# Kernel tuning notes

Hardware: AMD Instinct MI355X
Metric: run time of the kernel (lower is better)

Reference implementation:

```python
import jax, jax.numpy as jnp
import numpy as np

B, T, C, H, HS = 128, 256, 384, 6, 64
DFF = 4 * C
EPS = 1e-5


def layer_norm(x, g, b):
    mu = jnp.mean(x, axis=-1, keepdims=True)
    var = jnp.mean(jnp.square(x - mu), axis=-1, keepdims=True)
    return (x - mu) * jax.lax.rsqrt(var + EPS) * g + b


def setup_inputs() -> dict:
    key = jax.random.key(0)
    ks = jax.random.split(key, 12)
    s_in = 1.0 / np.sqrt(C)
    s_ff = 1.0 / np.sqrt(DFF)
    return {
        "x": jax.random.normal(ks[0], (B, T, C), jnp.float32),
        "Wq": jax.random.normal(ks[1], (H, C, HS), jnp.float32) * s_in,
        "Wk": jax.random.normal(ks[2], (H, C, HS), jnp.float32) * s_in,
        "Wv": jax.random.normal(ks[3], (H, C, HS), jnp.float32) * s_in,
        "Wo": jax.random.normal(ks[4], (C, C), jnp.float32) * s_in,
        "bo": jnp.zeros((C,), jnp.float32),
        "W1": jax.random.normal(ks[5], (C, DFF), jnp.float32) * s_in,
        "b1": jnp.zeros((DFF,), jnp.float32),
        "W2": jax.random.normal(ks[6], (DFF, C), jnp.float32) * s_ff,
        "b2": jnp.zeros((C,), jnp.float32),
        "g1": jnp.ones((C,), jnp.float32),
        "be1": jnp.zeros((C,), jnp.float32),
        "g2": jnp.ones((C,), jnp.float32),
        "be2": jnp.zeros((C,), jnp.float32),
    }


def reference(x, Wq, Wk, Wv, Wo, bo, W1, b1, W2, b2, g1, be1, g2, be2):
    # --- pre-norm causal multi-head self-attention (dropout = identity, eval mode) ---
    h = layer_norm(x, g1, be1)                      # (B,T,C)
    q = jnp.einsum('btc,hcd->bhtd', h, Wq)          # (B,H,T,HS)
    k = jnp.einsum('btc,hcd->bhtd', h, Wk)
    v = jnp.einsum('btc,hcd->bhtd', h, Wv)
    scale = HS ** -0.5
    wei = jnp.einsum('bhtd,bhsd->bhts', q, k) * scale   # (B,H,T,T)
    causal = jnp.tril(jnp.ones((T, T), bool))
    wei = jnp.where(causal, wei, -jnp.inf)
    wei = jax.nn.softmax(wei, axis=-1)
    attn = jnp.einsum('bhts,bhsd->bhtd', wei, v)         # (B,H,T,HS)
    attn = attn.transpose(0, 2, 1, 3).reshape(x.shape[0], x.shape[1], C)  # concat heads
    sa = attn @ Wo + bo
    x = x + sa
    # --- pre-norm FFN ---
    h2 = layer_norm(x, g2, be2)
    ff = jax.nn.relu(h2 @ W1 + b1) @ W2 + b2
    return x + ff
```

## Files before the change

kernel.cpp:

```cpp
#include <hip/hip_runtime.h>
#include <hip/hip_bf16.h>

#define BB   128
#define TT   256
#define CC   384
#define HH   6
#define HSZ  64
#define DFF  1536
#define EPSV 1e-5f
#define RPB  8
#define NTOK (BB * TT)
#define NQKV (3 * CC)

typedef __attribute__((ext_vector_type(8))) short  short8;
typedef __attribute__((ext_vector_type(4))) float  f32x4;
typedef __hip_bfloat16 bf16;

__device__ __forceinline__ void async_copy16(const bf16* g, bf16* l) {
    __builtin_amdgcn_global_load_lds(
        (const __attribute__((address_space(1))) void*)g,
        (__attribute__((address_space(3))) void*)l, 16, 0, 0);
}

__device__ __forceinline__ void block_reduce2(float& a, float& b, float* red) {
    #pragma unroll
    for (int off = 32; off > 0; off >>= 1) {
        a += __shfl_down(a, off, 64);
        b += __shfl_down(b, off, 64);
    }
    const int lane = threadIdx.x & 63;
    const int wid  = threadIdx.x >> 6;
    if (lane == 0) { red[wid * 2] = a; red[wid * 2 + 1] = b; }
    __syncthreads();
    if (threadIdx.x == 0) {
        float sa = 0.f, sb = 0.f;
        #pragma unroll
        for (int w = 0; w < 6; ++w) { sa += red[w * 2]; sb += red[w * 2 + 1]; }
        red[12] = sa; red[13] = sb;
    }
    __syncthreads();
    a = red[12]; b = red[13];
}

__global__ __launch_bounds__(CC) void ln_bf16_kernel(
        const float* __restrict__ x, const float* __restrict__ g,
        const float* __restrict__ be, bf16* __restrict__ y) {
    __shared__ float red[16];
    const int tid = threadIdx.x;
    const long row0 = (long)blockIdx.x * RPB;
    const float gg = g[tid], bb = be[tid];
    for (int r = 0; r < RPB; ++r) {
        float v = x[(row0 + r) * CC + tid];
        float s = v, sq = v * v;
        block_reduce2(s, sq, red);
        float mu  = s  * (1.0f / CC);
        float var = sq * (1.0f / CC) - mu * mu;
        float rs  = rsqrtf(var + EPSV);
        y[(row0 + r) * CC + tid] = __float2bfloat16((v - mu) * rs * gg + bb);
        __syncthreads();
    }
}

__global__ __launch_bounds__(256) void pack_weights(
        const float* __restrict__ Wq, const float* __restrict__ Wk,
        const float* __restrict__ Wv, const float* __restrict__ Wo,
        const float* __restrict__ W1, const float* __restrict__ W2,
        bf16* __restrict__ WcatT, bf16* __restrict__ WoT,
        bf16* __restrict__ W1T, bf16* __restrict__ W2T) {
    __shared__ float t[32][33];
    const int id = blockIdx.x;
    const float* in; bf16* out; int R, Cn, c0, r0;
    if (id < 432) {
        const int which = id / 144, rem = id % 144, h = rem / 24, tt = rem % 24;
        const float* W = (which == 0) ? Wq : ((which == 1) ? Wk : Wv);
        in = W + (long)h * CC * HSZ;  R = CC; Cn = HSZ;
        c0 = (tt % 2) * 32; r0 = (tt / 2) * 32;
        out = WcatT + ((long)which * CC + h * HSZ) * CC;
    } else if (id < 576) {
        const int i2 = id - 432;
        in = Wo; out = WoT; R = CC; Cn = CC;
        c0 = (i2 % 12) * 32; r0 = (i2 / 12) * 32;
    } else if (id < 1152) {
        const int i3 = id - 576;
        in = W1; out = W1T; R = CC; Cn = DFF;
        c0 = (i3 % 48) * 32; r0 = (i3 / 48) * 32;
    } else {
        const int i4 = id - 1152;
        in = W2; out = W2T; R = DFF; Cn = CC;
        c0 = (i4 % 12) * 32; r0 = (i4 / 12) * 32;
    }
    const int tid = threadIdx.x, tx = tid & 31, ty = tid >> 5;
    #pragma unroll
    for (int p = 0; p < 4; ++p)
        t[ty + p * 8][tx] = in[(long)(r0 + ty + p * 8) * Cn + c0 + tx];
    __syncthreads();
    #pragma unroll
    for (int p = 0; p < 4; ++p)
        out[(long)(c0 + ty + p * 8) * R + r0 + tx] = __float2bfloat16(t[tx][ty + p * 8]);
}

template<int K, int EPI>
__global__ __launch_bounds__(512) void gemm_fn(
        const bf16* __restrict__ A, const bf16* __restrict__ BT,
        const float* __restrict__ bias, const float* __restrict__ res,
        float* __restrict__ outF, bf16* __restrict__ outB, int N, int nby) {
    __shared__ bf16 A0[128 * 32];
    __shared__ bf16 A1[128 * 32];
    __shared__ bf16 B0[384 * 32];
    __shared__ bf16 B1[384 * 32];

    const int tid = threadIdx.x;

    const int hwid  = blockIdx.x;
    const int chunk = gridDim.x >> 3;
    const int e     = hwid & 7;
    const int s     = hwid >> 3;
    const int gx    = chunk / nby;
    const int bx    = e * gx + s / nby;
    const int by    = s - (s / nby) * nby;
    const int m0 = bx * 128;
    const int n0 = by * 384;

    const int ln   = tid & 63;
    const int wid  = tid >> 6;
    const int wm   = (wid & 1) * 64;
    const int wn   = (wid >> 1) * 96;
    const int fr   = ln & 15;
    const int quad = ln >> 4;
    const int slot = quad ^ ((fr >> 1) & 3);

    const int rA = tid >> 2, gA = (tid & 3) ^ ((rA >> 1) & 3);
    const long gaA = (long)rA * K + gA * 8;
    const int uB1 = tid + 512, uB2 = tid + 1024;
    const int rB0 = tid >> 2, gB0 = (tid & 3) ^ ((rB0 >> 1) & 3);
    const int rB1 = uB1 >> 2, gB1 = (uB1 & 3) ^ ((rB1 >> 1) & 3);
    const int rB2 = uB2 >> 2, gB2 = (uB2 & 3) ^ ((rB2 >> 1) & 3);
    const long gaB0 = (long)rB0 * K + gB0 * 8;
    const long gaB1 = (long)rB1 * K + gB1 * 8;
    const long gaB2 = (long)rB2 * K + gB2 * 8;
    const bf16* Ap  = A  + (long)m0 * K;
    const bf16* BTp = BT + (long)n0 * K;

    f32x4 acc[4][6];
    #pragma unroll
    for (int i = 0; i < 4; ++i)
        #pragma unroll
        for (int j = 0; j < 6; ++j)
            acc[i][j] = (f32x4){0.f, 0.f, 0.f, 0.f};

    constexpr int NT = K / 32;
    static_assert(NT % 2 == 0, "2-buffer rotation requires even NT");

    auto stage = [&](long k0, bf16* Ad, bf16* Bd) {
        async_copy16(Ap  + gaA  + k0, Ad + tid * 8);
        async_copy16(BTp + gaB0 + k0, Bd + tid * 8);
        async_copy16(BTp + gaB1 + k0, Bd + uB1 * 8);
        async_copy16(BTp + gaB2 + k0, Bd + uB2 * 8);
    };

    auto phase = [&](int t, bf16* Ab, bf16* Bb) {
        if (t + 1 < NT) {
            asm volatile("s_waitcnt vmcnt(4)" ::: "memory");
        } else {
            asm volatile("s_waitcnt vmcnt(0)" ::: "memory");
        }
        __builtin_amdgcn_s_barrier();

        short8 af[4], bfr[6];
        #pragma unroll
        for (int i = 0; i < 4; ++i)
            af[i] = *(const short8*)(Ab + (wm + i * 16 + fr) * 32 + slot * 8);
        #pragma unroll
        for (int j = 0; j < 6; ++j)
            bfr[j] = *(const short8*)(Bb + (wn + j * 16 + fr) * 32 + slot * 8);
        asm volatile("s_waitcnt lgkmcnt(0)" ::: "memory");
        __builtin_amdgcn_s_barrier();
        __builtin_amdgcn_sched_barrier(0);

        if (t + 2 < NT) stage((long)(t + 2) * 32, Ab, Bb);

        #pragma unroll
        for (int i = 0; i < 4; ++i)
            #pragma unroll
            for (int j = 0; j < 6; ++j)
                acc[i][j] = __builtin_amdgcn_mfma_f32_16x16x32_bf16(
                    af[i], bfr[j], acc[i][j], 0, 0, 0);
    };

    stage(0,  A0, B0);
    stage(32, A1, B1);

    for (int t = 0; t < NT; t += 2) {
        phase(t,     A0, B0);
        phase(t + 1, A1, B1);
    }

    #pragma unroll
    for (int i = 0; i < 4; ++i) {
        #pragma unroll
        for (int j = 0; j < 6; ++j) {
            const int col = n0 + wn + j * 16 + fr;
            #pragma unroll
            for (int r = 0; r < 4; ++r) {
                const int row = m0 + wm + i * 16 + quad * 4 + r;
                const long idx = (long)row * N + col;
                float v = acc[i][j][r];
                if (EPI == 1) {
                    v = fmaxf(v + bias[col], 0.f);
                    outB[idx] = __float2bfloat16(v);
                } else if (EPI == 2) {
                    outF[idx] = v + bias[col] + res[idx];
                } else {
                    outB[idx] = __float2bfloat16(v);
                }
            }
        }
    }
}

struct alignas(8) bh4s { bf16 a, b, c, d; };

__global__ __launch_bounds__(256, 2) void attn_mfma_kernel(
        const bf16* __restrict__ qkv, bf16* __restrict__ ab) {
    __shared__ bf16 Kt[64][72];
    __shared__ bf16 Vt[64][72];
    __shared__ bf16 Pb[4][16][72];

    const int tid  = threadIdx.x;
    const int bh   = blockIdx.x;
    const int b    = bh / HH, h = bh % HH;
    const int w    = tid >> 6;
    const int ln   = tid & 63;
    const int ln15 = ln & 15;
    const int quad = ln >> 4;

    short8 qf[4][2];
    #pragma unroll
    for (int i = 0; i < 4; ++i) {
        const long tok = (long)b * TT + w * 16 + i * 64 + ln15;
        const bf16* p = qkv + tok * NQKV + h * HSZ + quad * 8;
        qf[i][0] = *(const short8*)p;
        qf[i][1] = *(const short8*)(p + 32);
    }

    f32x4 accO[4][4];
    float mrow[4][4], lrow[4][4];
    #pragma unroll
    for (int i = 0; i < 4; ++i) {
        #pragma unroll
        for (int j = 0; j < 4; ++j) accO[i][j] = (f32x4){0.f, 0.f, 0.f, 0.f};
        #pragma unroll
        for (int r = 0; r < 4; ++r) { mrow[i][r] = -1e30f; lrow[i][r] = 0.f; }
    }

    for (int sidx = 0; sidx < 4; ++sidx) {
        const int s0 = sidx * 64;
        __syncthreads();
        {
            const bf16* kg = qkv + (long)(b * TT + s0) * NQKV + CC + h * HSZ;
            #pragma unroll
            for (int it = 0; it < 2; ++it) {
                const int u = tid + it * 256;
                const int r = u >> 3, c = (u & 7) * 8;
                *(uint4*)&Kt[r][c] = *(const uint4*)(kg + (long)r * NQKV + c);
            }
            const bf16* vg = qkv + (long)(b * TT + s0) * NQKV + 2 * CC + h * HSZ;
            const int s = tid & 63;
            #pragma unroll
            for (int it = 0; it < 4; ++it) {
                const int dq = (tid >> 6) + it * 4;
                const bh4s vv = *(const bh4s*)(vg + (long)s * NQKV + dq * 4);
                Vt[dq * 4 + 0][s] = vv.a;
                Vt[dq * 4 + 1][s] = vv.b;
                Vt[dq * 4 + 2][s] = vv.c;
                Vt[dq * 4 + 3][s] = vv.d;
            }
        }
        __syncthreads();

        #pragma unroll
        for (int i = 0; i < 4; ++i) {
            if (i < sidx) continue;
            const int rb = w * 16 + i * 64;
            f32x4 S[4];
            #pragma unroll
            for (int jt = 0; jt < 4; ++jt) S[jt] = (f32x4){0.f, 0.f, 0.f, 0.f};
            #pragma unroll
            for (int ks = 0; ks < 2; ++ks) {
                #pragma unroll
                for (int jt = 0; jt < 4; ++jt) {
                    const short8 kf = *(const short8*)&Kt[jt * 16 + ln15][ks * 32 + quad * 8];
                    S[jt] = __builtin_amdgcn_mfma_f32_16x16x32_bf16(qf[i][ks], kf, S[jt], 0, 0, 0);
                }
            }
            float rmax[4];
            #pragma unroll
            for (int r = 0; r < 4; ++r) rmax[r] = -1e30f;
            #pragma unroll
            for (int jt = 0; jt < 4; ++jt) {
                #pragma unroll
                for (int r = 0; r < 4; ++r) {
                    float v = S[jt][r] * 0.125f;
                    if (i == sidx) {
                        const int col = s0 + jt * 16 + ln15;
                        const int row = rb + quad * 4 + r;
                        if (col > row) v = -1e30f;
                    }
                    S[jt][r] = v;
                    rmax[r] = fmaxf(rmax[r], v);
                }
            }
            #pragma unroll
            for (int off = 1; off < 16; off <<= 1)
                #pragma unroll
                for (int r = 0; r < 4; ++r)
                    rmax[r] = fmaxf(rmax[r], __shfl_xor(rmax[r], off, 64));

            float alpha[4], rsum[4];
            #pragma unroll
            for (int r = 0; r < 4; ++r) {
                const float mn = fmaxf(mrow[i][r], rmax[r]);
                alpha[r] = __expf(mrow[i][r] - mn);
                mrow[i][r] = mn;
                rsum[r] = 0.f;
            }
            #pragma unroll
            for (int jt = 0; jt < 4; ++jt)
                #pragma unroll
                for (int r = 0; r < 4; ++r) {
                    const float p = __expf(S[jt][r] - mrow[i][r]);
                    S[jt][r] = p;
                    rsum[r] += p;
                }
            #pragma unroll
            for (int off = 1; off < 16; off <<= 1)
                #pragma unroll
                for (int r = 0; r < 4; ++r)
                    rsum[r] += __shfl_xor(rsum[r], off, 64);
            #pragma unroll
            for (int r = 0; r < 4; ++r)
                lrow[i][r] = lrow[i][r] * alpha[r] + rsum[r];
            #pragma unroll
            for (int jt = 0; jt < 4; ++jt)
                #pragma unroll
                for (int r = 0; r < 4; ++r)
                    accO[i][jt][r] *= alpha[r];

            #pragma unroll
            for (int jt = 0; jt < 4; ++jt)
                #pragma unroll
                for (int r = 0; r < 4; ++r)
                    Pb[w][quad * 4 + r][jt * 16 + ln15] = __float2bfloat16(S[jt][r]);
            const short8 pf0 = *(const short8*)&Pb[w][ln15][quad * 8];
            const short8 pf1 = *(const short8*)&Pb[w][ln15][32 + quad * 8];
            #pragma unroll
            for (int jt = 0; jt < 4; ++jt) {
                const short8 vf0 = *(const short8*)&Vt[jt * 16 + ln15][quad * 8];
                const short8 vf1 = *(const short8*)&Vt[jt * 16 + ln15][32 + quad * 8];
                accO[i][jt] = __builtin_amdgcn_mfma_f32_16x16x32_bf16(pf0, vf0, accO[i][jt], 0, 0, 0);
                accO[i][jt] = __builtin_amdgcn_mfma_f32_16x16x32_bf16(pf1, vf1, accO[i][jt], 0, 0, 0);
            }
        }
    }

    #pragma unroll
    for (int i = 0; i < 4; ++i) {
        const int rb = w * 16 + i * 64;
        float inv[4];
        #pragma unroll
        for (int r = 0; r < 4; ++r) inv[r] = 1.0f / lrow[i][r];
        #pragma unroll
        for (int jt = 0; jt < 4; ++jt)
            #pragma unroll
            for (int r = 0; r < 4; ++r)
                Pb[w][quad * 4 + r][jt * 16 + ln15] = __float2bfloat16(accO[i][jt][r] * inv[r]);
        #pragma unroll
        for (int it = 0; it < 2; ++it) {
            const int u = ln + it * 64;
            const int row = u >> 3, ch = (u & 7) * 8;
            const long tok = (long)b * TT + rb + row;
            *(uint4*)(ab + tok * CC + h * HSZ + ch) = *(const uint4*)&Pb[w][row][ch];
        }
    }
}

extern "C" void kernel_launch(void* const* d_in, const int* in_sizes, int n_in,
                              void* d_out, int out_size, void* d_ws, size_t ws_size,
                              hipStream_t stream) {
    const float* x   = (const float*)d_in[0];
    const float* Wq  = (const float*)d_in[1];
    const float* Wk  = (const float*)d_in[2];
    const float* Wv  = (const float*)d_in[3];
    const float* Wo  = (const float*)d_in[4];
    const float* bo  = (const float*)d_in[5];
    const float* W1  = (const float*)d_in[6];
    const float* b1  = (const float*)d_in[7];
    const float* W2  = (const float*)d_in[8];
    const float* b2  = (const float*)d_in[9];
    const float* g1  = (const float*)d_in[10];
    const float* be1 = (const float*)d_in[11];
    const float* g2  = (const float*)d_in[12];
    const float* be2 = (const float*)d_in[13];

    float* out = (float*)d_out;
    char*  ws  = (char*)d_ws;

    const size_t qkvBytes = (size_t)NTOK * NQKV * 4;
    const size_t actOff   = (qkvBytes + 255) & ~(size_t)255;
    const size_t actBytes = (size_t)NTOK * CC * 2;
    size_t wOff = (actOff + actBytes + 255) & ~(size_t)255;

    bf16* qkvb = (bf16*)ws;
    bf16* ff1  = (bf16*)ws;
    bf16* actb = (bf16*)(ws + actOff);

    bf16* WcatT = (bf16*)(ws + wOff); wOff += (size_t)NQKV * CC * 2 + 256;
    bf16* WoT   = (bf16*)(ws + ((wOff + 255) & ~(size_t)255)); wOff = ((wOff + 255) & ~(size_t)255) + (size_t)CC * CC * 2;
    bf16* W1T   = (bf16*)(ws + ((wOff + 255) & ~(size_t)255)); wOff = ((wOff + 255) & ~(size_t)255) + (size_t)DFF * CC * 2;
    bf16* W2T   = (bf16*)(ws + ((wOff + 255) & ~(size_t)255));

    pack_weights<<<1728, 256, 0, stream>>>(Wq, Wk, Wv, Wo, W1, W2,
                                           WcatT, WoT, W1T, W2T);

    ln_bf16_kernel<<<NTOK / RPB, CC, 0, stream>>>(x, g1, be1, actb);
    gemm_fn<CC, 3><<<(NTOK / 128) * 3, 512, 0, stream>>>(
        actb, WcatT, nullptr, nullptr, nullptr, qkvb, NQKV, 3);
    attn_mfma_kernel<<<BB * HH, 256, 0, stream>>>(qkvb, actb);
    gemm_fn<CC, 2><<<(NTOK / 128), 512, 0, stream>>>(
        actb, WoT, bo, x, out, nullptr, CC, 1);

    ln_bf16_kernel<<<NTOK / RPB, CC, 0, stream>>>(out, g2, be2, actb);
    gemm_fn<CC, 1><<<(NTOK / 128) * 4, 512, 0, stream>>>(
        actb, W1T, b1, nullptr, nullptr, ff1, DFF, 4);
    gemm_fn<DFF, 2><<<(NTOK / 128), 512, 0, stream>>>(
        ff1, W2T, b2, out, out, nullptr, CC, 1);
}
```

Baseline: 412.9 us.

## Fuse FFN up- and down-projection GEMMs into one kernel with LDS-resident hidden tile

Replaces the two FFN GEMM launches with one kernel. For each 128-row tile it computes 192-wide chunks of relu(h2·W1+b1), packs them as bf16 into shared memory, and immediately accumulates them into the W2 output with bias and residual. This removes the global write and reread of the large 32768x1536 intermediate and one launch. In exchange the grid is only 256 blocks of 512 threads with heavy LDS use and one block per CU, so occupancy is low and the pipeline schedule is intricate.

```diff
diff --git a/kernel.cpp b/kernel.cpp
--- a/kernel.cpp
+++ b/kernel.cpp
@@ -15,6 +15,11 @@
 typedef __attribute__((ext_vector_type(8))) short  short8;
 typedef __attribute__((ext_vector_type(4))) float  f32x4;
 typedef __hip_bfloat16 bf16;
+
+#define WAITV(n) asm volatile("s_waitcnt vmcnt(" #n ")" ::: "memory")
+#define WAITL    asm volatile("s_waitcnt lgkmcnt(0)" ::: "memory")
+#define BAR      __builtin_amdgcn_s_barrier()
+#define SCHED    __builtin_amdgcn_sched_barrier(0)
 
 __device__ __forceinline__ void async_copy16(const bf16* g, bf16* l) {
     __builtin_amdgcn_global_load_lds(
@@ -110,7 +115,6 @@
     __shared__ bf16 B1[384 * 32];
 
     const int tid = threadIdx.x;
-
     const int hwid  = blockIdx.x;
     const int chunk = gridDim.x >> 3;
     const int e     = hwid & 7;
@@ -149,7 +153,6 @@
             acc[i][j] = (f32x4){0.f, 0.f, 0.f, 0.f};
 
     constexpr int NT = K / 32;
-    static_assert(NT % 2 == 0, "2-buffer rotation requires even NT");
 
     auto stage = [&](long k0, bf16* Ad, bf16* Bd) {
         async_copy16(Ap  + gaA  + k0, Ad + tid * 8);
@@ -159,13 +162,8 @@
     };
 
     auto phase = [&](int t, bf16* Ab, bf16* Bb) {
-        if (t + 1 < NT) {
-            asm volatile("s_waitcnt vmcnt(4)" ::: "memory");
-        } else {
-            asm volatile("s_waitcnt vmcnt(0)" ::: "memory");
-        }
-        __builtin_amdgcn_s_barrier();
-
+        if (t + 1 < NT) { WAITV(4); } else { WAITV(0); }
+        BAR;
         short8 af[4], bfr[6];
         #pragma unroll
         for (int i = 0; i < 4; ++i)
@@ -173,12 +171,10 @@
         #pragma unroll
         for (int j = 0; j < 6; ++j)
             bfr[j] = *(const short8*)(Bb + (wn + j * 16 + fr) * 32 + slot * 8);
-        asm volatile("s_waitcnt lgkmcnt(0)" ::: "memory");
-        __builtin_amdgcn_s_barrier();
-        __builtin_amdgcn_sched_barrier(0);
-
+        WAITL;
+        BAR;
+        SCHED;
         if (t + 2 < NT) stage((long)(t + 2) * 32, Ab, Bb);
-
         #pragma unroll
         for (int i = 0; i < 4; ++i)
             #pragma unroll
@@ -205,14 +201,202 @@
                 const int row = m0 + wm + i * 16 + quad * 4 + r;
                 const long idx = (long)row * N + col;
                 float v = acc[i][j][r];
-                if (EPI == 1) {
-                    v = fmaxf(v + bias[col], 0.f);
-                    outB[idx] = __float2bfloat16(v);
-                } else if (EPI == 2) {
+                if (EPI == 2) {
                     outF[idx] = v + bias[col] + res[idx];
                 } else {
                     outB[idx] = __float2bfloat16(v);
                 }
+            }
+        }
+    }
+}
+
+__global__ __launch_bounds__(512, 1) void ffn_fused(
+        const bf16* __restrict__ A, const bf16* __restrict__ W1T,
+        const bf16* __restrict__ W2T, const float* __restrict__ b1,
+        const float* __restrict__ b2, float* __restrict__ out) {
+    __shared__ bf16 Pl[6 * 128 * 32];
+    __shared__ bf16 Ab0[2 * 128 * 32];
+    __shared__ bf16 Ab1[2 * 128 * 32];
+    __shared__ bf16 Bb0[1536 * 8];
+    __shared__ bf16 Bb1[1536 * 8];
+    __shared__ float b1L[DFF];
+    __shared__ float b2L[CC];
+
+    const int tid  = threadIdx.x;
+    const int hwid = blockIdx.x;
+    const int bx   = (hwid & 7) * 32 + (hwid >> 3);
+    const int m0   = bx * 128;
+
+    const int ln   = tid & 63;
+    const int wid  = tid >> 6;
+    const int wm   = (wid & 1) * 64;
+    const int wn1  = (wid >> 1) * 48;
+    const int wn2  = (wid >> 1) * 96;
+    const int fr   = ln & 15;
+    const int quad = ln >> 4;
+    const int sw8  = (quad ^ ((fr >> 1) & 3)) * 8;
+
+    for (int t = tid; t < DFF; t += 512) b1L[t] = b1[t];
+    for (int t = tid; t < CC;  t += 512) b2L[t] = b2[t];
+
+    const bf16* Ap = A + (long)m0 * CC;
+
+    auto stageA = [&](int s, bf16* Ad) {
+        #pragma unroll
+        for (int p = 0; p < 2; ++p) {
+            const int u = tid + p * 512;
+            const int kk = u >> 9, idx = u & 511;
+            const int row = idx >> 2, g = idx & 3;
+            const int gg = g ^ ((row >> 1) & 3);
+            async_copy16(Ap + (long)row * CC + s * 64 + kk * 32 + gg * 8,
+                         Ad + u * 8);
+        }
+    };
+    auto stageB1 = [&](int dffm, int s, bf16* Bd) {
+        #pragma unroll
+        for (int p = 0; p < 3; ++p) {
+            const int u = tid + p * 512;
+            const int sub = (u >= 768) ? 1 : 0;
+            const int idx = u - sub * 768;
+            const int row = idx >> 2, g = idx & 3;
+            const int gg = g ^ ((row >> 1) & 3);
+            async_copy16(W1T + (long)(dffm + row) * CC + s * 64 + sub * 32 + gg * 8,
+                         Bd + u * 8);
+        }
+    };
+    auto stageB2 = [&](int dffm, int uu, bf16* Bd) {
+        #pragma unroll
+        for (int p = 0; p < 3; ++p) {
+            const int u = tid + p * 512;
+            const int row = u >> 2, g = u & 3;
+            const int gg = g ^ ((row >> 1) & 3);
+            async_copy16(W2T + (long)row * DFF + dffm + uu * 32 + gg * 8,
+                         Bd + u * 8);
+        }
+    };
+
+    f32x4 acc1[4][3], acc2[4][6];
+    #pragma unroll
+    for (int i = 0; i < 4; ++i) {
+        #pragma unroll
+        for (int j = 0; j < 3; ++j) acc1[i][j] = (f32x4){0.f, 0.f, 0.f, 0.f};
+        #pragma unroll
+        for (int j = 0; j < 6; ++j) acc2[i][j] = (f32x4){0.f, 0.f, 0.f, 0.f};
+    }
+
+    auto g1phase = [&](const bf16* Ac, const bf16* Bc, int mode, int dffm,
+                       int aux, bf16* AD, bf16* BD) {
+        short8 af[4][2], bf1[3][2];
+        #pragma unroll
+        for (int kk = 0; kk < 2; ++kk) {
+            #pragma unroll
+            for (int i = 0; i < 4; ++i)
+                af[i][kk] = *(const short8*)(Ac + ((kk << 7) + wm + i * 16 + fr) * 32 + sw8);
+            #pragma unroll
+            for (int j = 0; j < 3; ++j)
+                bf1[j][kk] = *(const short8*)(Bc + (kk * 192 + wn1 + j * 16 + fr) * 32 + sw8);
+        }
+        WAITL;
+        BAR;
+        SCHED;
+        if (mode == 0) { stageA(aux, AD); stageB1(dffm, aux, BD); }
+        else if (mode == 1) { stageB2(dffm, aux, BD); }
+        #pragma unroll
+        for (int kk = 0; kk < 2; ++kk)
+            #pragma unroll
+            for (int i = 0; i < 4; ++i)
+                #pragma unroll
+                for (int j = 0; j < 3; ++j)
+                    acc1[i][j] = __builtin_amdgcn_mfma_f32_16x16x32_bf16(
+                        af[i][kk], bf1[j][kk], acc1[i][j], 0, 0, 0);
+    };
+    auto g2phase = [&](int uu, const bf16* Bc, int mode, int dffm,
+                       int aux, bf16* AD, bf16* BD) {
+        short8 af2[4], bf2[6];
+        #pragma unroll
+        for (int i = 0; i < 4; ++i)
+            af2[i] = *(const short8*)(Pl + (uu * 128 + wm + i * 16 + fr) * 32 + sw8);
+        #pragma unroll
+        for (int j = 0; j < 6; ++j)
+            bf2[j] = *(const short8*)(Bc + (wn2 + j * 16 + fr) * 32 + sw8);
+        WAITL;
+        BAR;
+        SCHED;
+        if (mode == 0) { stageA(aux, AD); stageB1(dffm, aux, BD); }
+        else if (mode == 1) { stageB2(dffm, aux, BD); }
+        #pragma unroll
+        for (int i = 0; i < 4; ++i)
+            #pragma unroll
+            for (int j = 0; j < 6; ++j)
+                acc2[i][j] = __builtin_amdgcn_mfma_f32_16x16x32_bf16(
+                    af2[i], bf2[j], acc2[i][j], 0, 0, 0);
+    };
+
+    __syncthreads();
+
+    stageA(0, Ab0); stageB1(0, 0, Bb0);
+    stageA(1, Ab1); stageB1(0, 1, Bb1);
+
+    for (int cc = 0; cc < 8; ++cc) {
+        const int dff0 = cc * 192;
+        const bool pf  = (cc < 7);
+        const int dffN = dff0 + 192;
+
+        WAITV(5); BAR; g1phase(Ab0, Bb0, 0, dff0, 2, Ab0, Bb0);
+        WAITV(5); BAR; g1phase(Ab1, Bb1, 0, dff0, 3, Ab1, Bb1);
+        WAITV(5); BAR; g1phase(Ab0, Bb0, 0, dff0, 4, Ab0, Bb0);
+        WAITV(5); BAR; g1phase(Ab1, Bb1, 0, dff0, 5, Ab1, Bb1);
+        WAITV(5); BAR; g1phase(Ab0, Bb0, 1, dff0, 0, nullptr, Bb0);
+        WAITV(3); BAR; g1phase(Ab1, Bb1, 1, dff0, 1, nullptr, Bb1);
+
+        #pragma unroll
+        for (int j = 0; j < 3; ++j) {
+            const float b1v = b1L[dff0 + wn1 + j * 16 + fr];
+            #pragma unroll
+            for (int i = 0; i < 4; ++i) {
+                #pragma unroll
+                for (int r = 0; r < 4; ++r) {
+                    const float v = fmaxf(acc1[i][j][r] + b1v, 0.f);
+                    const float pv = __shfl_xor(v, 1, 64);
+                    if (!(ln & 1)) {
+                        __hip_bfloat16 hl = __float2bfloat16(v);
+                        __hip_bfloat16 hh = __float2bfloat16(pv);
+                        const unsigned word =
+                            (unsigned)*(unsigned short*)&hl |
+                            ((unsigned)*(unsigned short*)&hh << 16);
+                        const int colC = wn1 + j * 16 + fr;
+                        const int row  = wm + i * 16 + quad * 4 + r;
+                        const int kt = colC >> 5, cl = colC & 31;
+                        const int phys = ((cl >> 3) ^ ((row >> 1) & 3)) * 8 + (cl & 7);
+                        *(unsigned*)((char*)Pl + ((kt * 128 + row) * 32 + phys) * 2) = word;
+                    }
+                    acc1[i][j][r] = 0.f;
+                }
+            }
+        }
+        WAITL;
+
+        WAITV(3); BAR; g2phase(0, Bb0, 1, dff0, 2, nullptr, Bb0);
+        WAITV(3); BAR; g2phase(1, Bb1, 1, dff0, 3, nullptr, Bb1);
+        WAITV(3); BAR; g2phase(2, Bb0, 1, dff0, 4, nullptr, Bb0);
+        WAITV(3); BAR; g2phase(3, Bb1, 1, dff0, 5, nullptr, Bb1);
+        WAITV(3); BAR; g2phase(4, Bb0, pf ? 0 : 2, dffN, 0, Ab0, Bb0);
+        if (pf) { WAITV(5); } else { WAITV(0); }
+        BAR;           g2phase(5, Bb1, pf ? 0 : 2, dffN, 1, Ab1, Bb1);
+    }
+
+    #pragma unroll
+    for (int i = 0; i < 4; ++i) {
+        #pragma unroll
+        for (int j = 0; j < 6; ++j) {
+            const int col = wn2 + j * 16 + fr;
+            const float b2v = b2L[col];
+            #pragma unroll
+            for (int r = 0; r < 4; ++r) {
+                const int row = m0 + wm + i * 16 + quad * 4 + r;
+                const long idx = (long)row * CC + col;
+                out[idx] = acc2[i][j][r] + b2v + out[idx];
             }
         }
     }
@@ -411,7 +595,6 @@
     size_t wOff = (actOff + actBytes + 255) & ~(size_t)255;
 
     bf16* qkvb = (bf16*)ws;
-    bf16* ff1  = (bf16*)ws;
     bf16* actb = (bf16*)(ws + actOff);
 
     bf16* WcatT = (bf16*)(ws + wOff); wOff += (size_t)NQKV * CC * 2 + 256;
@@ -430,8 +613,5 @@
         actb, WoT, bo, x, out, nullptr, CC, 1);
 
     ln_bf16_kernel<<<NTOK / RPB, CC, 0, stream>>>(out, g2, be2, actb);
-    gemm_fn<CC, 1><<<(NTOK / 128) * 4, 512, 0, stream>>>(
-        actb, W1T, b1, nullptr, nullptr, ff1, DFF, 4);
-    gemm_fn<DFF, 2><<<(NTOK / 128), 512, 0, stream>>>(
-        ff1, W2T, b2, out, out, nullptr, CC, 1);
-}
+    ffn_fused<<<256, 512, 0, stream>>>(actb, W1T, W2T, b1, b2, out);
+}
```

After: 505.9 us. +22.5%, slower.
